# Kernel tuning notes

Hardware: AMD Instinct MI355X
Metric: run time of the kernel (lower is better)

## Reference

```python
import jax, jax.numpy as jnp
import numpy as np

NT, NS, NH, NG, NR = 365, 256, 256, 32, 16
HID = 256


def setup_inputs() -> dict:
    key = jax.random.key(0)
    ks = jax.random.split(key, 8)
    s = 0.1  # keep exp() branches of sepPar well-scaled
    f32 = jnp.float32
    return {
        "x": jax.random.normal(ks[0], (NT, NS, 6), f32),
        "xc": jax.random.normal(ks[1], (NS, NG), f32),
        "fcW_w1": jax.random.normal(ks[2], (NG, HID), f32) * s,
        "fcW_b1": jnp.zeros((HID,), f32),
        "fcW_w2": jax.random.normal(ks[3], (HID, NH * 7), f32) * s,
        "fcW_b2": jnp.zeros((NH * 7,), f32),
        "fcT_w1": jax.random.normal(ks[4], (6 + NG, HID), f32) * s,
        "fcT_b1": jnp.zeros((HID,), f32),
        "fcT_w2": jax.random.normal(ks[5], (HID, NH * 3), f32) * s,
        "fcT_b2": jnp.zeros((NH * 3,), f32),
        "fcR_w1": jax.random.normal(ks[6], (NG, HID), f32) * s,
        "fcR_b1": jnp.zeros((HID,), f32),
        "fcR_w2": jax.random.normal(ks[7], (HID, NH * NR), f32) * s,
        "fcR_b2": jnp.zeros((NH * NR,), f32),
    }


def _forward(x, xc, fcW_w1, fcW_b1, fcW_w2, fcW_b2, fcT_w1, fcT_b1, fcT_w2, fcT_b2,
             fcR_w1, fcR_b1, fcR_w2, fcR_b2):
    nt, ns, _ = x.shape
    nh, nr = NH, NR
    P, E, T1, T2 = x[..., 0], x[..., 1], x[..., 2], x[..., 3]

    mlp = lambda a, w1, b1, w2, b2: jnp.tanh(a @ w1 + b1) @ w2 + b2  # dropout = eval identity
    seg = lambda p, k: p[..., nh * k:nh * (k + 1)]

    # --- fcW -> per-basin reservoir params (wLst: sig,sig,sig,sig,exp,relu,skip) ---
    w = mlp(xc, fcW_w1, fcW_b1, fcW_w2, fcW_b2)            # [ns, nh*7]
    kp = jax.nn.sigmoid(seg(w, 0))
    ks_ = jax.nn.sigmoid(seg(w, 1))
    kg = jax.nn.sigmoid(seg(w, 2)) / 10.0
    gp = jax.nn.sigmoid(seg(w, 3))
    gL = jnp.exp(seg(w, 4)) ** 2
    qb = jax.nn.relu(seg(w, 5))
    ga = jax.nn.softmax(seg(w, 6), axis=-1)                # [ns, nh]

    # --- fcT -> per-timestep params (vLst: skip,relu,exp) ---
    xcT = jnp.concatenate([x, jnp.broadcast_to(xc[None], (nt, ns, xc.shape[-1]))], axis=-1)
    v = mlp(xcT, fcT_w1, fcT_b1, fcT_w2, fcT_b2)           # [nt, ns, nh*3]
    vi = jnp.clip(seg(v, 0) * 2.0 / 6.0 + 0.5, 0.0, 1.0)   # hardsigmoid(vi*2)
    ve = jax.nn.relu(seg(v, 1)) * 2.0
    vm = jnp.exp(seg(v, 2))

    # --- fcR -> routing (unit hydrograph) weights ---
    rf = jax.nn.relu(mlp(xc, fcR_w1, fcR_b1, fcR_w2, fcR_b2))  # [ns, nh*nr]

    # --- forwardPreQ: snow/liquid partition by temperature ---
    ratio = jnp.clip((T1 + T2) / (T2 - T1), -1.0, 1.0)
    vf = jnp.arccos(ratio) / 3.1415
    vf = jnp.where(T1 >= 0, 0.0, vf)
    vf = jnp.where(T2 <= 0, 1.0, vf)
    Ps = P * vf                                             # [nt, ns] snowfall
    Pl = (P * (1.0 - vf))[:, :, None] * vi                  # [nt, ns, nh]
    Ev = E[:, :, None] * ve                                 # [nt, ns, nh]

    # --- sequential reservoir routing (forwardStepQ) via lax.scan ---
    def step(carry, inp):
        Sf, Ss, Sg = carry
        fs, fl, fev, fm = inp
        qf = jnp.minimum(Sf + fs, fm)
        Sf = jax.nn.relu(Sf + fs - fm)
        H = jax.nn.relu(Ss + fl + qf - fev)
        qp = jax.nn.relu(kp * (H - gL))
        qsa = ks_ * jnp.minimum(H, gL)
        Ss = H - qp - qsa
        qsg = qsa * gp
        qs = qsa * (1.0 - gp)
        qg = kg * (Sg + qsg) + qb
        Sg = (1.0 - kg) * (Sg + qsg) - qb
        return (Sf, Ss, Sg), qp + qs + qg

    S0 = jnp.zeros((ns, nh), x.dtype)
    _, Q = jax.lax.scan(step, (S0, S0, S0), (Ps[:, :, None], Pl, Ev, vm))  # Q: [nt, ns, nh]

    # --- convTS: depthwise valid cross-correlation with softmax kernel ---
    # conv is linear and Qp/Qs/Qg share the same kernel, so conv(Qp)+conv(Qs)+conv(Qg)=conv(Qp+Qs+Qg)
    r = jax.nn.softmax(rf.reshape(ns, nh, nr), axis=-1)
    T = nt - nr + 1
    y = r[:, :, 0] * Q[0:T]
    for j in range(1, nr):  # small fixed nr taps
        y = y + r[:, :, j] * Q[j:j + T]

    return jnp.sum(y * ga, axis=2)  # [nt-nr+1, ns]


def reference(x, xc, fcW_w1, fcW_b1, fcW_w2, fcW_b2, fcT_w1, fcT_b1, fcT_w2, fcT_b2,
              fcR_w1, fcR_b1, fcR_w2, fcR_b2):
    return _forward(x, xc, fcW_w1, fcW_b1, fcW_w2, fcW_b2, fcT_w1, fcT_b1, fcT_w2, fcT_b2,
                    fcR_w1, fcR_b1, fcR_w2, fcR_b2)
```

## Files before the change

### kernel.cpp

```cpp
#include <hip/hip_runtime.h>

#define NT   365
#define NS   256
#define NH   256
#define NG   32
#define NR   16
#define HID  256
#define NX   38
#define M_   (NT*NS)
#define TOUT (NT-NR+1)

typedef __attribute__((ext_vector_type(8))) short short8;
typedef __attribute__((ext_vector_type(4))) float floatx4;
typedef unsigned short u16;

__device__ __forceinline__ u16 f2bf(float f) {
    unsigned u = __float_as_uint(f);
    u = (u + 0x7FFFu + ((u >> 16) & 1u)) >> 16;
    return (u16)u;
}
__device__ __forceinline__ float sigmoidf_(float x) { return 1.f / (1.f + __expf(-x)); }


__global__ __launch_bounds__(256) void k_prep(const float* __restrict__ x,
                                              float* __restrict__ psT, float* __restrict__ plcT,
                                              float* __restrict__ e2T, float* __restrict__ out,
                                              const float* __restrict__ tw2, u16* __restrict__ w2tT,
                                              const float* __restrict__ fw2, u16* __restrict__ w2tW,
                                              const float* __restrict__ rw2, u16* __restrict__ w2tR,
                                              const float* __restrict__ xc,
                                              const float* __restrict__ wW, const float* __restrict__ bW,
                                              const float* __restrict__ wR, const float* __restrict__ bR,
                                              u16* __restrict__ h1W, u16* __restrict__ h1R) {
    int bx = blockIdx.x, tid = threadIdx.x;
    if (bx < 365) {
        int m = bx * 256 + tid;
        if (m < TOUT*NS) out[m] = 0.f;
        float P  = x[m*6+0], E = x[m*6+1], T1 = x[m*6+2], T2 = x[m*6+3];
        float vf;
        if (T2 <= 0.f)      vf = 1.f;
        else if (T1 >= 0.f) vf = 0.f;
        else {
            float ratio = (T1 + T2) / (T2 - T1);
            ratio = fminf(fmaxf(ratio, -1.f), 1.f);
            vf = acosf(ratio) * (1.f / 3.1415f);
        }
        psT[tid*368 + bx]  = P * vf;
        plcT[tid*368 + bx] = P * (1.f - vf);
        e2T[tid*368 + bx]  = 2.f * E;
    } else if (bx < 781) {
        __shared__ u16 tile[64][65];
        int i2 = bx - 365;
        int bn_ = i2 % 104, bk = i2 / 104;
        const float* w; u16* wt; int N, bn; bool frag;
        if (bn_ < 12)      { w = tw2; wt = w2tT; N = 768;  bn = bn_;      frag = true;  }
        else if (bn_ < 40) { w = fw2; wt = w2tW; N = 1792; bn = bn_ - 12; frag = false; }
        else               { w = rw2; wt = w2tR; N = 4096; bn = bn_ - 40; frag = false; }
        for (int i = tid; i < 64*64; i += 256) {
            int kk = i >> 6, nn = i & 63;
            tile[nn][kk] = f2bf(w[(size_t)(bk*64 + kk)*N + bn*64 + nn]);
        }
        __syncthreads();
        for (int i = tid; i < 64*64; i += 256) {
            int nn = i >> 6, kk = i & 63;
            int n = bn*64 + nn, k = bk*64 + kk;
            if (frag) {
                int ntile = n >> 4, kg = k >> 5;
                int lane2 = (n & 15) | (((k & 31) >> 3) << 4);
                wt[(((size_t)(ntile*8 + kg)) << 9) + (lane2 << 3) + (k & 7)] = tile[nn][kk];
            } else {
                wt[(size_t)n*256 + k] = tile[nn][kk];
            }
        }
    } else {
        int b = bx - 781;
        int net = b >> 4, grp = b & 15;
        const float* w1 = net ? wR : wW;
        const float* b1 = net ? bR : bW;
        u16* o = net ? h1R : h1W;
        int s0 = grp * 16, j = tid;
        __shared__ float xs1[16][NG];
        for (int i = j; i < 16*NG; i += 256) xs1[i >> 5][i & 31] = xc[s0*NG + i];
        __syncthreads();
        float acc[16];
        float bb = b1[j];
#pragma unroll
        for (int si = 0; si < 16; ++si) acc[si] = bb;
        for (int g = 0; g < NG; ++g) {
            float w = w1[g*HID + j];
#pragma unroll
            for (int si = 0; si < 16; ++si) acc[si] += xs1[si][g] * w;
        }
#pragma unroll
        for (int si = 0; si < 16; ++si) o[(s0 + si)*256 + j] = f2bf(tanhf(acc[si]));
    }
}

__global__ __launch_bounds__(256) void k_mid(const u16* __restrict__ h1W, const u16* __restrict__ w2tW,
                                             const float* __restrict__ fb2, float* __restrict__ wlog,
                                             const u16* __restrict__ h1R, const u16* __restrict__ w2tR,
                                             const float* __restrict__ rb2, float* __restrict__ rbuf,
                                             const float* __restrict__ x, const float* __restrict__ xc,
                                             const float* __restrict__ tw1, const float* __restrict__ tb1,
                                             u16* __restrict__ h1b) {
    int bx = blockIdx.x, tid = threadIdx.x;
    if (bx < 92) {
        int mode, bm, bn, Nn;
        const u16 *A, *B; const float* bias; float* outp;
        if (bx < 28) { mode = 0; bm = bx % 2;        bn = bx / 2;        Nn = 1792; A = h1W; B = w2tW; bias = fb2; outp = wlog; }
        else         { mode = 1; bm = (bx - 28) % 2; bn = (bx - 28) / 2; Nn = 4096; A = h1R; B = w2tR; bias = rb2; outp = rbuf; }
        int wave = tid >> 6, lane = tid & 63;
        __shared__ __align__(16) u16 As[128*32];
        __shared__ __align__(16) u16 Bs[128*32];
        floatx4 acc[4][4];
#pragma unroll
        for (int i = 0; i < 4; ++i)
#pragma unroll
            for (int jj = 0; jj < 4; ++jj) acc[i][jj] = (floatx4)(0.f);
        int m0 = bm*128, n0 = bn*128;
        int rA = tid >> 2, cA = (tid & 3) * 8;
        int wm = (wave >> 1)*64, wn = (wave & 1)*64, lr = lane & 15, lq = lane >> 4;
        for (int k0 = 0; k0 < 256; k0 += 32) {
            short8 a0  = *(const short8*)(A + (m0 + rA     )*256 + k0 + cA);
            short8 a1  = *(const short8*)(A + (m0 + rA + 64)*256 + k0 + cA);
            short8 bv0 = *(const short8*)(B + (n0 + rA     )*256 + k0 + cA);
            short8 bv1 = *(const short8*)(B + (n0 + rA + 64)*256 + k0 + cA);
            __syncthreads();
            *(short8*)(As + rA*32 + cA)        = a0;
            *(short8*)(As + (rA + 64)*32 + cA) = a1;
            *(short8*)(Bs + rA*32 + cA)        = bv0;
            *(short8*)(Bs + (rA + 64)*32 + cA) = bv1;
            __syncthreads();
            short8 af[4], bf[4];
#pragma unroll
            for (int i = 0; i < 4; ++i)
                af[i] = *(const short8*)(As + (wm + i*16 + lr)*32 + lq*8);
#pragma unroll
            for (int jj = 0; jj < 4; ++jj)
                bf[jj] = *(const short8*)(Bs + (wn + jj*16 + lr)*32 + lq*8);
#pragma unroll
            for (int i = 0; i < 4; ++i)
#pragma unroll
                for (int jj = 0; jj < 4; ++jj)
                    acc[i][jj] = __builtin_amdgcn_mfma_f32_16x16x32_bf16(af[i], bf[jj], acc[i][jj], 0, 0, 0);
        }
#pragma unroll
        for (int jj = 0; jj < 4; ++jj) {
            int n_glob = n0 + wn + jj*16 + lr;
            float bv = bias[n_glob];
            int hg = (n0 + wn + jj*16) >> 4;
#pragma unroll
            for (int i = 0; i < 4; ++i) {
#pragma unroll
                for (int rr = 0; rr < 4; ++rr) {
                    int m = m0 + wm + i*16 + lq*4 + rr;
                    float v = acc[i][jj][rr] + bv;
                    if (mode == 0) {
                        outp[(size_t)m*Nn + n_glob] = v;
                    } else {
                        v = fmaxf(v, 0.f);
                        float mx = v;
#pragma unroll
                        for (int d = 1; d < 16; d <<= 1) mx = fmaxf(mx, __shfl_xor(mx, d, 64));
                        float e = __expf(v - mx);
                        float sm = e;
#pragma unroll
                        for (int d = 1; d < 16; d <<= 1) sm += __shfl_xor(sm, d, 64);
                        outp[(size_t)m*4096 + hg*16 + lr] = e / sm;
                    }
                }
            }
        }
    } else {
        int m0 = (bx - 92) * 32;
        int j = tid;
        __shared__ float xs[32][NX + 2];
        __shared__ __align__(16) u16 hs[32][264];
        for (int idx = j; idx < 32*NX; idx += 256) {
            int rr = idx / NX, c = idx % NX;
            int m = m0 + rr;
            int mc = m < M_ ? m : M_ - 1;
            int s = mc & (NS - 1);
            xs[rr][c] = (c < 6) ? x[mc*6 + c] : xc[s*NG + (c - 6)];
        }
        __syncthreads();
        float acc[32];
        float b = tb1[j];
#pragma unroll
        for (int rr = 0; rr < 32; ++rr) acc[rr] = b;
        for (int g = 0; g < NX; ++g) {
            float w = tw1[g*HID + j];
#pragma unroll
            for (int rr = 0; rr < 32; ++rr) acc[rr] += xs[rr][g] * w;
        }
#pragma unroll
        for (int rr = 0; rr < 32; ++rr) hs[rr][j] = f2bf(tanhf(acc[rr]));
        __syncthreads();
        int t_  = m0 >> 8;
        int tt_ = t_ >> 4, tr_ = t_ & 15;
        int s0_ = m0 & 255;
#pragma unroll
        for (int p = 0; p < 4; ++p) {
            int cid = p*256 + tid;
            int rr = cid >> 5, c = cid & 31;
            int kg = c >> 2, lh = c & 3;
            int j0 = kg*32 + lh*8;
            short8 v = *(const short8*)(&hs[rr][j0]);
            *(short8*)(h1b + (size_t)(s0_ + rr)*94208
                       + (((size_t)tt_*8 + kg) << 9)
                       + ((tr_ | (lh << 4)) << 3)) = v;
        }
    }
}

__global__ __launch_bounds__(256) void k_post(const float* __restrict__ wlog,
                                              float* __restrict__ par) {
    __shared__ float red[256];
    int s = blockIdx.x, j = threadIdx.x;
    const float* L = wlog + (size_t)s*1792;
    float o0 = L[j], o1 = L[256+j], o2 = L[512+j], o3 = L[768+j],
          o4 = L[1024+j], o5 = L[1280+j], o6 = L[1536+j];
    red[j] = o6; __syncthreads();
    for (int st = 128; st > 0; st >>= 1) {
        if (j < st) red[j] = fmaxf(red[j], red[j+st]);
        __syncthreads();
    }
    float mx = red[0]; __syncthreads();
    float e = __expf(o6 - mx);
    red[j] = e; __syncthreads();
    for (int st = 128; st > 0; st >>= 1) {
        if (j < st) red[j] += red[j+st];
        __syncthreads();
    }
    float ga = e / red[0];
    int idx = s*NH + j;
    par[0*65536 + idx] = sigmoidf_(o0);
    par[1*65536 + idx] = sigmoidf_(o1);
    par[2*65536 + idx] = 0.1f * sigmoidf_(o2);
    par[3*65536 + idx] = sigmoidf_(o3);
    par[4*65536 + idx] = __expf(2.f * o4);
    par[5*65536 + idx] = fmaxf(o5, 0.f);
    par[6*65536 + idx] = ga;
}

__global__ __launch_bounds__(64, 1) void k_scanfuse(const u16* __restrict__ h1b,
                                                    const u16* __restrict__ w2t,
                                                    const float* __restrict__ b2,
                                                    const float* __restrict__ psT,
                                                    const float* __restrict__ plcT,
                                                    const float* __restrict__ e2T,
                                                    const float* __restrict__ par,
                                                    const float* __restrict__ r,
                                                    float* __restrict__ out) {
    int bx = blockIdx.x;
    int xcd = bx & 7, local = bx >> 3;
    int sgrp = xcd*8 + (local >> 4);
    int hb = local & 15;
    int lane = threadIdx.x;
    int h_idx = lane & 15, s_idx = lane >> 4;
    int s_g = sgrp*4 + s_idx, h_g = hb*16 + h_idx;
    int pidx = s_g*NH + h_g;

    __shared__ float s_ps[4][368];
    __shared__ float s_plc[4][368];
    __shared__ float s_e2[4][368];
    __shared__ float xbuf[4*872];

#pragma unroll
    for (int si = 0; si < 4; ++si) {
        int sg = sgrp*4 + si;
        for (int t = lane; t < 368; t += 64) {
            bool v = (t < NT);
            s_ps[si][t]  = v ? psT[sg*368 + t]  : 0.f;
            s_plc[si][t] = v ? plcT[sg*368 + t] : 0.f;
            s_e2[si][t]  = v ? e2T[sg*368 + t]  : 0.f;
        }
    }

    float kp = par[pidx], ks_ = par[65536+pidx], kg = par[2*65536+pidx],
          gp = par[3*65536+pidx], gL = par[4*65536+pidx], qb = par[5*65536+pidx],
          ga = par[6*65536+pidx];
    float rt[NR];
#pragma unroll
    for (int k = 0; k < NR; ++k) rt[k] = r[(size_t)pidx*NR + k] * ga;
    float bias0 = b2[0*256 + h_g], bias1 = b2[1*256 + h_g], bias2 = b2[2*256 + h_g];

    short8 Bv[3][8];
#pragma unroll
    for (int sg2 = 0; sg2 < 3; ++sg2)
#pragma unroll
        for (int kgi = 0; kgi < 8; ++kgi)
            Bv[sg2][kgi] = *(const short8*)(w2t + (((size_t)((sg2*16 + hb)*8 + kgi)) << 9) + (lane << 3));

    const u16* Ab = h1b + (size_t)(sgrp*4)*94208 + (lane << 3);
    short8 Av[4][8];
#pragma unroll
    for (int si = 0; si < 4; ++si)
#pragma unroll
        for (int kgi = 0; kgi < 8; ++kgi)
            Av[si][kgi] = *(const short8*)(Ab + (size_t)si*94208 + kgi*512);

    __syncthreads();

    float Sf = 0.f, Ss = 0.f, Sg = 0.f;
    float qwin[16];
#pragma unroll
    for (int k = 0; k < 16; ++k) qwin[k] = 0.f;
    float* sredp = xbuf;

    for (int blk = 0; blk < 23; ++blk) {
        int tbase = blk * 16;
        floatx4 acc[4][3];
#pragma unroll
        for (int si = 0; si < 4; ++si)
#pragma unroll
            for (int sg2 = 0; sg2 < 3; ++sg2) acc[si][sg2] = (floatx4)(0.f);
#pragma unroll
        for (int kgi = 0; kgi < 8; ++kgi)
#pragma unroll
            for (int si = 0; si < 4; ++si)
#pragma unroll
                for (int sg2 = 0; sg2 < 3; ++sg2)
                    acc[si][sg2] = __builtin_amdgcn_mfma_f32_16x16x32_bf16(Av[si][kgi], Bv[sg2][kgi], acc[si][sg2], 0, 0, 0);
        if (blk < 22) {
            const u16* An = Ab + (size_t)(blk+1)*4096;
#pragma unroll
            for (int si = 0; si < 4; ++si)
#pragma unroll
                for (int kgi = 0; kgi < 8; ++kgi)
                    Av[si][kgi] = *(const short8*)(An + (size_t)si*94208 + kgi*512);
        }
        __builtin_amdgcn_sched_barrier(0);
#pragma unroll
    for (int si = 0; si < 4; ++si) {
#pragma unroll
            for (int rr = 0; rr < 4; ++rr) {
                int trow = s_idx*4 + rr;
                int t = tbase + trow;
                float v0 = acc[si][0][rr] + bias0;
                float v1 = acc[si][1][rr] + bias1;
                float v2 = acc[si][2][rr] + bias2;
                float pl = s_plc[si][t] * fminf(fmaxf(v0*(1.f/3.f) + 0.5f, 0.f), 1.f);
                float ev = s_e2[si][t] * fmaxf(v1, 0.f);
                float fm = __expf(v2);
                xbuf[si*872 + 0*288 + trow*18 + h_idx] = pl;
                xbuf[si*872 + 1*288 + trow*18 + h_idx] = ev;
                xbuf[si*872 + 2*288 + trow*18 + h_idx] = fm;
            }
        }
        __syncthreads();
        float cv[16];
#pragma unroll
        for (int j = 0; j < 16; ++j) cv[j] = 0.f;
#pragma unroll
        for (int j = 0; j < 16; ++j) {
            int t = tbase + j;
            if (t < NT) {
                float pl = xbuf[s_idx*872 + 0*288 + j*18 + h_idx];
                float ev = xbuf[s_idx*872 + 1*288 + j*18 + h_idx];
                float fm = xbuf[s_idx*872 + 2*288 + j*18 + h_idx];
                float fs = s_ps[s_idx][t];
                float qf = fminf(Sf + fs, fm);
                Sf = fmaxf(Sf + fs - fm, 0.f);
                float H = fmaxf(Ss + pl + qf - ev, 0.f);
                float qp = fmaxf(kp * (H - gL), 0.f);
                float qsa = ks_ * fminf(H, gL);
                Ss = H - qp - qsa;
                float qsg = qsa * gp;
                float qs = qsa - qsg;
                float qg = kg * (Sg + qsg) + qb;
                Sg = (1.f - kg) * (Sg + qsg) - qb;
                float q = qp + qs + qg;
                qwin[j] = q;
                if (t >= 15) {
                    float c = 0.f;
#pragma unroll
                    for (int k = 0; k < 16; ++k) c += rt[k] * qwin[(j + 1 + k) & 15];
                    cv[j] = c;
                }
            }
        }
        __syncthreads();
#pragma unroll
        for (int j = 0; j < 16; ++j) sredp[j*65 + lane] = cv[j];
        __syncthreads();
        {
            int j2 = lane & 15, q2 = lane >> 4;
            float p = 0.f;
#pragma unroll
            for (int i = 0; i < 16; ++i) p += sredp[j2*65 + q2*16 + i];
            int tout = tbase + j2 - 15;
            if (tout >= 0 && tout < TOUT)
                atomicAdd(out + tout*NS + sgrp*4 + q2, p);
        }
        __syncthreads();
    }
}

extern "C" void kernel_launch(void* const* d_in, const int* in_sizes, int n_in,
                              void* d_out, int out_size, void* d_ws, size_t ws_size,
                              hipStream_t stream) {
    const float* x   = (const float*)d_in[0];
    const float* xc  = (const float*)d_in[1];
    const float* fw1 = (const float*)d_in[2];
    const float* fb1 = (const float*)d_in[3];
    const float* fw2 = (const float*)d_in[4];
    const float* fb2 = (const float*)d_in[5];
    const float* tw1 = (const float*)d_in[6];
    const float* tb1 = (const float*)d_in[7];
    const float* tw2 = (const float*)d_in[8];
    const float* tb2 = (const float*)d_in[9];
    const float* rw1 = (const float*)d_in[10];
    const float* rb1 = (const float*)d_in[11];
    const float* rw2 = (const float*)d_in[12];
    const float* rb2 = (const float*)d_in[13];
    float* out = (float*)d_out;
    char* ws = (char*)d_ws;

    constexpr size_t OFF_PS    = 0;
    constexpr size_t OFF_PLC   = 376832;
    constexpr size_t OFF_E2    = 753664;
    constexpr size_t OFF_PAR   = 1130496;
    constexpr size_t OFF_R     = 2965504;
    constexpr size_t OFF_W2TT  = 7159808;
    constexpr size_t OFF_H1B   = 7553024;
    constexpr size_t OFF_PC    = 55787520;
    constexpr size_t OFF_WLOG  = 200491008;
    constexpr size_t OFF_W2TW  = OFF_PC + 0;
    constexpr size_t OFF_W2TR  = OFF_PC + 917504;
    constexpr size_t OFF_H1W   = OFF_PC + 3014656;
    constexpr size_t OFF_H1R   = OFF_PC + 3145728;

    float* psT   = (float*)(ws + OFF_PS);
    float* plcT  = (float*)(ws + OFF_PLC);
    float* e2T   = (float*)(ws + OFF_E2);
    float* par   = (float*)(ws + OFF_PAR);
    float* rbuf  = (float*)(ws + OFF_R);
    u16*   w2tT  = (u16*)(ws + OFF_W2TT);
    u16*   h1b   = (u16*)(ws + OFF_H1B);
    float* wlog  = (float*)(ws + OFF_WLOG);
    u16*   w2tW  = (u16*)(ws + OFF_W2TW);
    u16*   w2tR  = (u16*)(ws + OFF_W2TR);
    u16*   h1W   = (u16*)(ws + OFF_H1W);
    u16*   h1R   = (u16*)(ws + OFF_H1R);

    k_prep     <<<813, 256, 0, stream>>>(x, psT, plcT, e2T, out,
                                         tw2, w2tT, fw2, w2tW, rw2, w2tR,
                                         xc, fw1, fb1, rw1, rb1, h1W, h1R);
    k_mid      <<<3036, 256, 0, stream>>>(h1W, w2tW, fb2, wlog,
                                          h1R, w2tR, rb2, rbuf,
                                          x, xc, tw1, tb1, h1b);
    k_post     <<<256, 256, 0, stream>>>(wlog, par);
    k_scanfuse <<<1024, 64, 0, stream>>>(h1b, w2tT, tb2, psT, plcT, e2T, par, rbuf, out);
}
```

Measured before the change: 299.3 us.

## Split scan kernel into producer MFMA wave and consumer scan wave with double buffering

The fused scan kernel now runs two waves per block. Wave 0 computes the fcT second-layer MFMA and activation for chunk k+1 into one half of a double-buffered LDS area, while wave 1 runs the sequential reservoir scan and routing convolution on chunk k. The goal is to overlap the matrix work with the serial recurrence, which previously ran one after the other within a single wave. The cost is an extra barrier per chunk, more LDS, and A operands that are now loaded per k-slice without prefetching. plc/e2 are also read straight from global memory instead of being staged in LDS.

```diff
diff --git a/kernel.cpp b/kernel.cpp
--- a/kernel.cpp
+++ b/kernel.cpp
@@ -243,155 +243,155 @@
     par[6*65536 + idx] = ga;
 }
 
-__global__ __launch_bounds__(64, 1) void k_scanfuse(const u16* __restrict__ h1b,
-                                                    const u16* __restrict__ w2t,
-                                                    const float* __restrict__ b2,
-                                                    const float* __restrict__ psT,
-                                                    const float* __restrict__ plcT,
-                                                    const float* __restrict__ e2T,
-                                                    const float* __restrict__ par,
-                                                    const float* __restrict__ r,
-                                                    float* __restrict__ out) {
+__global__ __launch_bounds__(128, 2) void k_scanfuse(const u16* __restrict__ h1b,
+                                                     const u16* __restrict__ w2t,
+                                                     const float* __restrict__ b2,
+                                                     const float* __restrict__ psT,
+                                                     const float* __restrict__ plcT,
+                                                     const float* __restrict__ e2T,
+                                                     const float* __restrict__ par,
+                                                     const float* __restrict__ r,
+                                                     float* __restrict__ out) {
     int bx = blockIdx.x;
     int xcd = bx & 7, local = bx >> 3;
     int sgrp = xcd*8 + (local >> 4);
     int hb = local & 15;
-    int lane = threadIdx.x;
+    int tid = threadIdx.x;
+    int wv = tid >> 6;
+    int lane = tid & 63;
     int h_idx = lane & 15, s_idx = lane >> 4;
     int s_g = sgrp*4 + s_idx, h_g = hb*16 + h_idx;
     int pidx = s_g*NH + h_g;
 
     __shared__ float s_ps[4][368];
-    __shared__ float s_plc[4][368];
-    __shared__ float s_e2[4][368];
-    __shared__ float xbuf[4*872];
-
-#pragma unroll
-    for (int si = 0; si < 4; ++si) {
-        int sg = sgrp*4 + si;
-        for (int t = lane; t < 368; t += 64) {
-            bool v = (t < NT);
-            s_ps[si][t]  = v ? psT[sg*368 + t]  : 0.f;
-            s_plc[si][t] = v ? plcT[sg*368 + t] : 0.f;
-            s_e2[si][t]  = v ? e2T[sg*368 + t]  : 0.f;
-        }
-    }
-
-    float kp = par[pidx], ks_ = par[65536+pidx], kg = par[2*65536+pidx],
-          gp = par[3*65536+pidx], gL = par[4*65536+pidx], qb = par[5*65536+pidx],
-          ga = par[6*65536+pidx];
+    __shared__ float xbuf[2][4*872];
+    __shared__ float sred[16*65];
+
+    for (int i = tid; i < 4*368; i += 128) {
+        int si = i / 368, t = i % 368;
+        s_ps[si][t] = (t < NT) ? psT[(sgrp*4 + si)*368 + t] : 0.f;
+    }
+
+    short8 Bv[3][8];
+    float bias0 = 0.f, bias1 = 0.f, bias2 = 0.f;
+    const u16* Ab = h1b + (size_t)(sgrp*4)*94208 + (lane << 3);
+    float kp = 0.f, ks_ = 0.f, kg = 0.f, gp = 0.f, gL = 0.f, qb = 0.f;
     float rt[NR];
-#pragma unroll
-    for (int k = 0; k < NR; ++k) rt[k] = r[(size_t)pidx*NR + k] * ga;
-    float bias0 = b2[0*256 + h_g], bias1 = b2[1*256 + h_g], bias2 = b2[2*256 + h_g];
-
-    short8 Bv[3][8];
-#pragma unroll
-    for (int sg2 = 0; sg2 < 3; ++sg2)
-#pragma unroll
-        for (int kgi = 0; kgi < 8; ++kgi)
-            Bv[sg2][kgi] = *(const short8*)(w2t + (((size_t)((sg2*16 + hb)*8 + kgi)) << 9) + (lane << 3));
-
-    const u16* Ab = h1b + (size_t)(sgrp*4)*94208 + (lane << 3);
-    short8 Av[4][8];
-#pragma unroll
-    for (int si = 0; si < 4; ++si)
-#pragma unroll
-        for (int kgi = 0; kgi < 8; ++kgi)
-            Av[si][kgi] = *(const short8*)(Ab + (size_t)si*94208 + kgi*512);
-
-    __syncthreads();
-
     float Sf = 0.f, Ss = 0.f, Sg = 0.f;
     float qwin[16];
 #pragma unroll
-    for (int k = 0; k < 16; ++k) qwin[k] = 0.f;
-    float* sredp = xbuf;
-
-    for (int blk = 0; blk < 23; ++blk) {
-        int tbase = blk * 16;
+    for (int k = 0; k < 16; ++k) { qwin[k] = 0.f; rt[k] = 0.f; }
+
+    if (wv == 0) {
+#pragma unroll
+        for (int sg2 = 0; sg2 < 3; ++sg2)
+#pragma unroll
+            for (int kgi = 0; kgi < 8; ++kgi)
+                Bv[sg2][kgi] = *(const short8*)(w2t + (((size_t)((sg2*16 + hb)*8 + kgi)) << 9) + (lane << 3));
+        bias0 = b2[0*256 + h_g]; bias1 = b2[1*256 + h_g]; bias2 = b2[2*256 + h_g];
+    } else {
+        kp = par[pidx]; ks_ = par[65536+pidx]; kg = par[2*65536+pidx];
+        gp = par[3*65536+pidx]; gL = par[4*65536+pidx]; qb = par[5*65536+pidx];
+        float ga = par[6*65536+pidx];
+#pragma unroll
+        for (int k = 0; k < NR; ++k) rt[k] = r[(size_t)pidx*NR + k] * ga;
+    }
+
+    auto produce = [&](int c, int b) {
+        int tbase = c * 16;
         floatx4 acc[4][3];
 #pragma unroll
         for (int si = 0; si < 4; ++si)
 #pragma unroll
             for (int sg2 = 0; sg2 < 3; ++sg2) acc[si][sg2] = (floatx4)(0.f);
-#pragma unroll
-        for (int kgi = 0; kgi < 8; ++kgi)
+        const u16* An = Ab + (size_t)c*4096;
+#pragma unroll
+        for (int kgi = 0; kgi < 8; ++kgi) {
+            short8 Avk[4];
 #pragma unroll
             for (int si = 0; si < 4; ++si)
+                Avk[si] = *(const short8*)(An + (size_t)si*94208 + kgi*512);
+#pragma unroll
+            for (int si = 0; si < 4; ++si)
 #pragma unroll
                 for (int sg2 = 0; sg2 < 3; ++sg2)
-                    acc[si][sg2] = __builtin_amdgcn_mfma_f32_16x16x32_bf16(Av[si][kgi], Bv[sg2][kgi], acc[si][sg2], 0, 0, 0);
-        if (blk < 22) {
-            const u16* An = Ab + (size_t)(blk+1)*4096;
-#pragma unroll
-            for (int si = 0; si < 4; ++si)
-#pragma unroll
-                for (int kgi = 0; kgi < 8; ++kgi)
-                    Av[si][kgi] = *(const short8*)(An + (size_t)si*94208 + kgi*512);
-        }
-        __builtin_amdgcn_sched_barrier(0);
-#pragma unroll
-    for (int si = 0; si < 4; ++si) {
+                    acc[si][sg2] = __builtin_amdgcn_mfma_f32_16x16x32_bf16(Avk[si], Bv[sg2][kgi], acc[si][sg2], 0, 0, 0);
+        }
+        float* xb = &xbuf[b][0];
+#pragma unroll
+        for (int si = 0; si < 4; ++si) {
+            int sg = sgrp*4 + si;
+            floatx4 plv = *(const floatx4*)(plcT + sg*368 + tbase + s_idx*4);
+            floatx4 e2v = *(const floatx4*)(e2T  + sg*368 + tbase + s_idx*4);
 #pragma unroll
             for (int rr = 0; rr < 4; ++rr) {
                 int trow = s_idx*4 + rr;
-                int t = tbase + trow;
                 float v0 = acc[si][0][rr] + bias0;
                 float v1 = acc[si][1][rr] + bias1;
                 float v2 = acc[si][2][rr] + bias2;
-                float pl = s_plc[si][t] * fminf(fmaxf(v0*(1.f/3.f) + 0.5f, 0.f), 1.f);
-                float ev = s_e2[si][t] * fmaxf(v1, 0.f);
+                float pl = plv[rr] * fminf(fmaxf(v0*(1.f/3.f) + 0.5f, 0.f), 1.f);
+                float ev = e2v[rr] * fmaxf(v1, 0.f);
                 float fm = __expf(v2);
-                xbuf[si*872 + 0*288 + trow*18 + h_idx] = pl;
-                xbuf[si*872 + 1*288 + trow*18 + h_idx] = ev;
-                xbuf[si*872 + 2*288 + trow*18 + h_idx] = fm;
+                xb[si*872 + 0*288 + trow*18 + h_idx] = pl;
+                xb[si*872 + 1*288 + trow*18 + h_idx] = ev;
+                xb[si*872 + 2*288 + trow*18 + h_idx] = fm;
             }
         }
-        __syncthreads();
-        float cv[16];
-#pragma unroll
-        for (int j = 0; j < 16; ++j) cv[j] = 0.f;
-#pragma unroll
-        for (int j = 0; j < 16; ++j) {
-            int t = tbase + j;
-            if (t < NT) {
-                float pl = xbuf[s_idx*872 + 0*288 + j*18 + h_idx];
-                float ev = xbuf[s_idx*872 + 1*288 + j*18 + h_idx];
-                float fm = xbuf[s_idx*872 + 2*288 + j*18 + h_idx];
-                float fs = s_ps[s_idx][t];
-                float qf = fminf(Sf + fs, fm);
-                Sf = fmaxf(Sf + fs - fm, 0.f);
-                float H = fmaxf(Ss + pl + qf - ev, 0.f);
-                float qp = fmaxf(kp * (H - gL), 0.f);
-                float qsa = ks_ * fminf(H, gL);
-                Ss = H - qp - qsa;
-                float qsg = qsa * gp;
-                float qs = qsa - qsg;
-                float qg = kg * (Sg + qsg) + qb;
-                Sg = (1.f - kg) * (Sg + qsg) - qb;
-                float q = qp + qs + qg;
-                qwin[j] = q;
-                if (t >= 15) {
-                    float c = 0.f;
-#pragma unroll
-                    for (int k = 0; k < 16; ++k) c += rt[k] * qwin[(j + 1 + k) & 15];
-                    cv[j] = c;
+    };
+
+    __syncthreads();
+    if (wv == 0) produce(0, 0);
+    __syncthreads();
+
+    for (int k = 0; k < 23; ++k) {
+        if (wv == 0) {
+            if (k < 22) produce(k + 1, (k + 1) & 1);
+        } else {
+            int tbase = k * 16;
+            const float* xr = &xbuf[k & 1][0];
+            float cv[16];
+#pragma unroll
+            for (int j = 0; j < 16; ++j) cv[j] = 0.f;
+#pragma unroll
+            for (int j = 0; j < 16; ++j) {
+                int t = tbase + j;
+                if (t < NT) {
+                    float pl = xr[s_idx*872 + 0*288 + j*18 + h_idx];
+                    float ev = xr[s_idx*872 + 1*288 + j*18 + h_idx];
+                    float fm = xr[s_idx*872 + 2*288 + j*18 + h_idx];
+                    float fs = s_ps[s_idx][t];
+                    float qf = fminf(Sf + fs, fm);
+                    Sf = fmaxf(Sf + fs - fm, 0.f);
+                    float H = fmaxf(Ss + pl + qf - ev, 0.f);
+                    float qp = fmaxf(kp * (H - gL), 0.f);
+                    float qsa = ks_ * fminf(H, gL);
+                    Ss = H - qp - qsa;
+                    float qsg = qsa * gp;
+                    float qs = qsa - qsg;
+                    float qg = kg * (Sg + qsg) + qb;
+                    Sg = (1.f - kg) * (Sg + qsg) - qb;
+                    float q = qp + qs + qg;
+                    qwin[j] = q;
+                    if (t >= 15) {
+                        float c = 0.f;
+#pragma unroll
+                        for (int kk = 0; kk < 16; ++kk) c += rt[kk] * qwin[(j + 1 + kk) & 15];
+                        cv[j] = c;
+                    }
                 }
             }
-        }
-        __syncthreads();
-#pragma unroll
-        for (int j = 0; j < 16; ++j) sredp[j*65 + lane] = cv[j];
-        __syncthreads();
-        {
-            int j2 = lane & 15, q2 = lane >> 4;
-            float p = 0.f;
-#pragma unroll
-            for (int i = 0; i < 16; ++i) p += sredp[j2*65 + q2*16 + i];
-            int tout = tbase + j2 - 15;
-            if (tout >= 0 && tout < TOUT)
-                atomicAdd(out + tout*NS + sgrp*4 + q2, p);
+#pragma unroll
+            for (int j = 0; j < 16; ++j) sred[j*65 + lane] = cv[j];
+            asm volatile("s_waitcnt lgkmcnt(0)" ::: "memory");
+            {
+                int j2 = lane & 15, q2 = lane >> 4;
+                float p = 0.f;
+#pragma unroll
+                for (int i = 0; i < 16; ++i) p += sred[j2*65 + q2*16 + i];
+                int tout = tbase + j2 - 15;
+                if (tout >= 0 && tout < TOUT)
+                    atomicAdd(out + tout*NS + sgrp*4 + q2, p);
+            }
         }
         __syncthreads();
     }
@@ -451,5 +451,5 @@
                                           h1R, w2tR, rb2, rbuf,
                                           x, xc, tw1, tb1, h1b);
     k_post     <<<256, 256, 0, stream>>>(wlog, par);
-    k_scanfuse <<<1024, 64, 0, stream>>>(h1b, w2tT, tb2, psT, plcT, e2T, par, rbuf, out);
-}
+    k_scanfuse <<<1024, 128, 0, stream>>>(h1b, w2tT, tb2, psT, plcT, e2T, par, rbuf, out);
+}
```

Measured after the change: 298.2 us. Within noise of the previous version (-0.4%).
